# Kernel tuning notes

Hardware: AMD Instinct MI355X
Metric: run time of the kernel (lower is better)

Reference implementation:

```python
import math
import jax, jax.numpy as jnp
import numpy as np

B, S, D, H = 2, 2048, 2048, 16
HD = D // H
EPS = 1e-6


def _precompute_freqs_cis(dim, end, theta=500000.0):
    inv_freqs = 1.0 / theta ** (np.arange(0, dim, 2, dtype=np.float32) / dim)
    t = np.arange(end, dtype=np.float32)
    freqs = np.outer(t, inv_freqs).astype(np.float32)
    # [1, end, 1, dim//2, 2] matching torch stack(cos, sin, dim=4)
    return jnp.asarray(np.stack([np.cos(freqs)[None, :, None, :], np.sin(freqs)[None, :, None, :]], axis=4))


def setup_inputs() -> dict:
    key = jax.random.key(0)
    k1, k2, k3 = jax.random.split(key, 3)
    x = jax.random.normal(k1, (B, S, D), dtype=jnp.float32)
    w_qkv = jax.random.normal(k2, (3 * D, D), dtype=jnp.float32) * 0.02
    w_out = jax.random.normal(k3, (D, D), dtype=jnp.float32) * 0.02
    attn_scale = jnp.asarray(math.log2(S * S - S), dtype=jnp.float32)
    freqs_cis = _precompute_freqs_cis(HD, S)
    return {"x": x, "w_qkv": w_qkv, "w_out": w_out, "attn_scale": attn_scale, "freqs_cis": freqs_cis}


def _apply_rotary(q, k, fc):
    # q, k: [b, s, h, hd]; fc: [1, s, 1, hd//2, 2]
    b, s, h, hd = q.shape
    qk = jnp.concatenate([q, k], axis=2).reshape(b, s, 2 * h, hd // 2, 2)
    real = qk[..., 0] * fc[..., 0] - qk[..., 1] * fc[..., 1]
    imag = qk[..., 1] * fc[..., 0] + qk[..., 0] * fc[..., 1]
    rot = jnp.stack([real, imag], axis=-1).reshape(b, s, 2 * h, hd)
    return rot[:, :, :h], rot[:, :, h:]


def reference(x, w_qkv, w_out, attn_scale, freqs_cis):
    b, s, d = x.shape
    qkv = x @ w_qkv.T                      # [b, s, 3d]
    q, k, v = jnp.split(qkv, 3, axis=2)
    q = q.reshape(b, s, H, HD)
    k = k.reshape(b, s, H, HD)
    v = v.reshape(b, s, H, HD)
    q, k = _apply_rotary(q, k, freqs_cis[:, :s])
    # -> [b, h, s, hd]
    q = q.transpose(0, 2, 1, 3)
    k = k.transpose(0, 2, 1, 3)
    v = v.transpose(0, 2, 1, 3)
    # per-head L2 norm of q/k, learned scale on q
    q = q / (jnp.linalg.norm(q, axis=-1, keepdims=True) + EPS)
    k = k / (jnp.linalg.norm(k, axis=-1, keepdims=True) + EPS)
    q = q * attn_scale
    # causal SDPA with scale=1.0
    scores = jnp.einsum('bhqd,bhkd->bhqk', q, k)
    causal = jnp.tril(jnp.ones((s, s), dtype=bool))
    scores = jnp.where(causal, scores, -jnp.inf)
    attn = jax.nn.softmax(scores, axis=-1)
    out = jnp.einsum('bhqk,bhkd->bhqd', attn, v)
    out = out.transpose(0, 2, 1, 3).reshape(b, s, d)
    return out @ w_out.T
```

## Files before the change

kernel.cpp:

```cpp
#include <hip/hip_runtime.h>
#include <stdint.h>

#define B_  2
#define S_  2048
#define D_  2048
#define H_  16
#define HD_ 128
#define D3_ 6144

typedef unsigned short u16;
typedef __attribute__((ext_vector_type(8))) __bf16 bf16x8;
typedef __attribute__((ext_vector_type(4))) float f32x4;
typedef __attribute__((ext_vector_type(8))) u16  u16x8;
typedef __attribute__((ext_vector_type(4))) u16  u16x4;
typedef __attribute__((ext_vector_type(2))) u16  u16x2;

__device__ inline u16 f2bf(float f) {
  union { float f; uint32_t u; } v; v.f = f;
  uint32_t r = v.u + 0x7FFFu + ((v.u >> 16) & 1u);
  return (u16)(r >> 16);
}
__device__ inline float bf2f(u16 u) {
  union { float f; uint32_t u; } v; v.u = ((uint32_t)u) << 16;
  return v.f;
}
__device__ inline void gload_lds16(const void* g, void* l) {
  __builtin_amdgcn_global_load_lds((const __attribute__((address_space(1))) uint32_t*)g,
                                   (__attribute__((address_space(3))) uint32_t*)l, 16, 0, 0);
}

#define TILE_SYNC() do { \
    asm volatile("s_waitcnt lgkmcnt(0)" ::: "memory"); \
    asm volatile("s_waitcnt vmcnt(0)" ::: "memory"); \
    __builtin_amdgcn_s_barrier(); \
    asm volatile("" ::: "memory"); \
  } while (0)

__global__ __launch_bounds__(256) void castk(const float* __restrict__ in, u16* __restrict__ out, int n) {
  int i = blockIdx.x * 256 + threadIdx.x;
  int n8 = n >> 3;
  if (i < n8) {
    f32x4 a = ((const f32x4*)in)[2*i];
    f32x4 b = ((const f32x4*)in)[2*i + 1];
    u16x8 o;
#pragma unroll
    for (int j = 0; j < 4; ++j) o[j] = f2bf(a[j]);
#pragma unroll
    for (int j = 0; j < 4; ++j) o[4+j] = f2bf(b[j]);
    ((u16x8*)out)[i] = o;
  }
}

template<int BF16OUT>
__global__ __launch_bounds__(512, 2) void gemm8(const u16* __restrict__ A, const u16* __restrict__ Bw,
                                                void* __restrict__ Cp, int M, int N, int K) {
  __shared__ __align__(16) u16 lds_[65536];
  char* ldsb = (char*)lds_;
  const int tid = threadIdx.x;
  const int w = tid >> 6, l = tid & 63;
  const int lr = l & 15, lg = l >> 4;
  const int wr = w >> 2, wc = w & 3;
  const int nbn = (int)gridDim.x;
  const int nwg = nbn * (int)gridDim.y;
  const int bid = (int)(blockIdx.y * gridDim.x + blockIdx.x);
  const int swz = (bid & 7) * (nwg >> 3) + (bid >> 3);
  const int bm = swz / nbn, bn = swz % nbn;

  f32x4 acc[8][4] = {};

  int row4[4], col4[4];
#pragma unroll
  for (int i = 0; i < 4; ++i) {
    int off = i*8192 + tid*16;
    row4[i] = off >> 7;
    col4[i] = (off & 127) ^ ((row4[i] & 7) << 4);
  }
  const size_t rs = (size_t)K * 2;
  const char* Ab = (const char*)A + (size_t)bm * 256 * rs;
  const char* Bb = (const char*)Bw + (size_t)bn * 256 * rs;
  const int wb = w * 1024;

#define STG(T_) do { \
    char* dA_ = ldsb + ((T_)&1)*32768; \
    char* dB_ = ldsb + 65536 + ((T_)&1)*32768; \
    _Pragma("unroll") \
    for (int i_ = 0; i_ < 4; ++i_) \
      gload_lds16(Ab + (size_t)row4[i_]*rs + (size_t)(T_)*128 + col4[i_], dA_ + i_*8192 + wb); \
    _Pragma("unroll") \
    for (int i_ = 0; i_ < 4; ++i_) \
      gload_lds16(Bb + (size_t)row4[i_]*rs + (size_t)(T_)*128 + col4[i_], dB_ + i_*8192 + wb); \
  } while (0)

#define RD_A(dst, mf, ks) do { int row_ = wr*128 + (mf)*16 + lr; \
    dst = *(const bf16x8*)(La + row_*128 + (((ks)*64 + lg*16) ^ ((row_ & 7) << 4))); } while (0)
#define RD_B(dst, nf, ks) do { int row_ = wc*64 + (nf)*16 + lr; \
    dst = *(const bf16x8*)(Lb + row_*128 + (((ks)*64 + lg*16) ^ ((row_ & 7) << 4))); } while (0)

  const int NT = K >> 6;
  STG(0);
  TILE_SYNC();

  for (int T = 0; T < NT; ++T) {
    const char* La = ldsb + (T & 1)*32768;
    const char* Lb = ldsb + 65536 + (T & 1)*32768;
    if (T + 1 < NT) STG(T + 1);

    bf16x8 a0[8], a1[8], b0[4], b1[4];
#pragma unroll
    for (int mf = 0; mf < 8; ++mf) { RD_A(a0[mf], mf, 0); RD_A(a1[mf], mf, 1); }
#pragma unroll
    for (int nf = 0; nf < 4; ++nf) { RD_B(b0[nf], nf, 0); RD_B(b1[nf], nf, 1); }
#pragma unroll
    for (int mf = 0; mf < 8; ++mf)
#pragma unroll
      for (int nf = 0; nf < 4; ++nf)
        acc[mf][nf] = __builtin_amdgcn_mfma_f32_16x16x32_bf16(a0[mf], b0[nf], acc[mf][nf], 0, 0, 0);
#pragma unroll
    for (int mf = 0; mf < 8; ++mf)
#pragma unroll
      for (int nf = 0; nf < 4; ++nf)
        acc[mf][nf] = __builtin_amdgcn_mfma_f32_16x16x32_bf16(a1[mf], b1[nf], acc[mf][nf], 0, 0, 0);
    TILE_SYNC();
  }
#undef STG
#undef RD_A
#undef RD_B

#pragma unroll
  for (int mf = 0; mf < 8; ++mf)
#pragma unroll
    for (int nf = 0; nf < 4; ++nf)
#pragma unroll
      for (int j = 0; j < 4; ++j) {
        int m = bm*256 + wr*128 + mf*16 + lg*4 + j;
        int n = bn*256 + wc*64 + nf*16 + lr;
        float v = acc[mf][nf][j];
        if (BF16OUT) ((u16*)Cp)[(size_t)m * N + n] = f2bf(v);
        else         ((float*)Cp)[(size_t)m * N + n] = v;
      }
}

template<int BF16OUT>
__global__ __launch_bounds__(256, 2) void gemm_bt(const u16* __restrict__ A, const u16* __restrict__ Bw,
                                                  void* __restrict__ Cp, int M, int N, int K) {
  __shared__ __align__(16) u16 lds_[32768];
  char* ldsb = (char*)lds_;
  const int tid = threadIdx.x;
  const int w = tid >> 6, l = tid & 63;
  const int lr = l & 15, lg = l >> 4;
  const int nwg = (int)(gridDim.x * gridDim.y);
  const int bid = (int)(blockIdx.y * gridDim.x + blockIdx.x);
  const int swz = (bid & 7) * (nwg >> 3) + (bid >> 3);
  const int bm = swz / (int)gridDim.x, bn = swz % (int)gridDim.x;
  const int wr = w >> 1, wc = w & 1;

  f32x4 acc[4][4] = {};

  int row4[4], col4[4];
#pragma unroll
  for (int i = 0; i < 4; ++i) {
    int off = i*4096 + tid*16;
    row4[i] = off >> 7;
    col4[i] = (off & 127) ^ ((row4[i] & 7) << 4);
  }
  const size_t rs = (size_t)K * 2;
  const char* Ab = (const char*)A + (size_t)bm * 128 * rs;
  const char* Bb = (const char*)Bw + (size_t)bn * 128 * rs;
  const int wb = w * 1024;

#define STG(T_) do { \
    char* dA_ = ldsb + ((T_)&1)*16384; \
    char* dB_ = ldsb + 32768 + ((T_)&1)*16384; \
    _Pragma("unroll") \
    for (int i_ = 0; i_ < 4; ++i_) \
      gload_lds16(Ab + (size_t)row4[i_]*rs + (size_t)(T_)*128 + col4[i_], dA_ + i_*4096 + wb); \
    _Pragma("unroll") \
    for (int i_ = 0; i_ < 4; ++i_) \
      gload_lds16(Bb + (size_t)row4[i_]*rs + (size_t)(T_)*128 + col4[i_], dB_ + i_*4096 + wb); \
  } while (0)

  const int NT = K >> 6;
  STG(0);
  TILE_SYNC();

  for (int T = 0; T < NT; ++T) {
    const char* La = ldsb + (T & 1)*16384;
    const char* Lb = ldsb + 32768 + (T & 1)*16384;
    if (T + 1 < NT) STG(T + 1);

    bf16x8 af[4][2], bf[4][2];
#pragma unroll
    for (int mt = 0; mt < 4; ++mt) {
      int row = wr*64 + mt*16 + lr;
#pragma unroll
      for (int ks = 0; ks < 2; ++ks)
        af[mt][ks] = *(const bf16x8*)(La + row*128 + ((ks*64 + lg*16) ^ ((row & 7) << 4)));
    }
#pragma unroll
    for (int nt = 0; nt < 4; ++nt) {
      int row = wc*64 + nt*16 + lr;
#pragma unroll
      for (int ks = 0; ks < 2; ++ks)
        bf[nt][ks] = *(const bf16x8*)(Lb + row*128 + ((ks*64 + lg*16) ^ ((row & 7) << 4)));
    }
#pragma unroll
    for (int mt = 0; mt < 4; ++mt)
#pragma unroll
      for (int nt = 0; nt < 4; ++nt)
        acc[mt][nt] = __builtin_amdgcn_mfma_f32_16x16x32_bf16(af[mt][0], bf[nt][0], acc[mt][nt], 0, 0, 0);
#pragma unroll
    for (int mt = 0; mt < 4; ++mt)
#pragma unroll
      for (int nt = 0; nt < 4; ++nt)
        acc[mt][nt] = __builtin_amdgcn_mfma_f32_16x16x32_bf16(af[mt][1], bf[nt][1], acc[mt][nt], 0, 0, 0);
    TILE_SYNC();
  }
#undef STG

#pragma unroll
  for (int mt = 0; mt < 4; ++mt)
#pragma unroll
    for (int nt = 0; nt < 4; ++nt)
#pragma unroll
      for (int j = 0; j < 4; ++j) {
        int m = bm*128 + wr*64 + mt*16 + lg*4 + j;
        int n = bn*128 + wc*64 + nt*16 + lr;
        float v = acc[mt][nt][j];
        if (BF16OUT) ((u16*)Cp)[(size_t)m * N + n] = f2bf(v);
        else         ((float*)Cp)[(size_t)m * N + n] = v;
      }
}

__global__ __launch_bounds__(256) void rope_norm(const u16* __restrict__ qkv, const float* __restrict__ fc,
                                                 const float* __restrict__ scale_p,
                                                 u16* __restrict__ Qo, u16* __restrict__ Ko) {
  int gid = blockIdx.x;
  int bs = gid >> 2;
  int s = bs & (S_ - 1);
  int b = bs >> 11;
  int w = threadIdx.x >> 6, l = threadIdx.x & 63;
  int h = (gid & 3)*4 + w;
  float2 cs = ((const float2*)fc)[(size_t)s*64 + l];
  float scale = scale_p[0] * 1.4426950408889634f;
  const u16* base = qkv + (size_t)bs * D3_;
  size_t obase = ((size_t)(b*H_ + h) * S_ + s) * HD_ + 2*l;
  {
    const u16* p = base + h*HD_ + 2*l;
    float x0 = bf2f(p[0]), x1 = bf2f(p[1]);
    float r0 = x0*cs.x - x1*cs.y;
    float r1 = x1*cs.x + x0*cs.y;
    float t = r0*r0 + r1*r1;
#pragma unroll
    for (int mk = 1; mk < 64; mk <<= 1) t += __shfl_xor(t, mk, 64);
    float inv = scale / (sqrtf(t) + 1e-6f);
    u16x2 o; o[0] = f2bf(r0*inv); o[1] = f2bf(r1*inv);
    *(u16x2*)(Qo + obase) = o;
  }
  {
    const u16* p = base + D_ + h*HD_ + 2*l;
    float x0 = bf2f(p[0]), x1 = bf2f(p[1]);
    float r0 = x0*cs.x - x1*cs.y;
    float r1 = x1*cs.x + x0*cs.y;
    float t = r0*r0 + r1*r1;
#pragma unroll
    for (int mk = 1; mk < 64; mk <<= 1) t += __shfl_xor(t, mk, 64);
    float inv = 1.0f / (sqrtf(t) + 1e-6f);
    u16x2 o; o[0] = f2bf(r0*inv); o[1] = f2bf(r1*inv);
    *(u16x2*)(Ko + obase) = o;
  }
}

__global__ __launch_bounds__(256) void v_trans(const u16* __restrict__ qkv, u16* __restrict__ Vt) {
  __shared__ u16 vt[64][136];
  int blk = blockIdx.x;
  int bh = blk >> 5, st = blk & 31;
  int b = bh >> 4, h = bh & 15;
  int s0 = st * 64;
  int tid = threadIdx.x;
#pragma unroll
  for (int i = 0; i < 4; ++i) {
    int idx = tid + i*256;
    int row = idx >> 4, ch = idx & 15;
    u16x8 v = *(const u16x8*)(qkv + (size_t)(b*S_ + s0 + row) * D3_ + 2*D_ + h*HD_ + ch*8);
    *(u16x8*)(&vt[row][ch*8]) = v;
  }
  __syncthreads();
#pragma unroll
  for (int p = 0; p < 2; ++p) {
    int d = p*64 + (tid >> 2);
    int q = (tid & 3) * 16;
    u16x8 t0, t1;
#pragma unroll
    for (int i = 0; i < 8; ++i) t0[i] = vt[q + i][d];
#pragma unroll
    for (int i = 0; i < 8; ++i) t1[i] = vt[q + 8 + i][d];
    u16* dst = Vt + ((size_t)bh * HD_ + d) * S_ + s0 + q;
    *(u16x8*)dst = t0;
    *(u16x8*)(dst + 8) = t1;
  }
}

__global__ __launch_bounds__(512) void flash_attn(const u16* __restrict__ Qh, const u16* __restrict__ Kh,
                                                  const u16* __restrict__ Vt, u16* __restrict__ AO) {
  __shared__ __align__(16) u16 lK[2][64*128];
  __shared__ __align__(16) u16 lV[128*64];
  __shared__ __align__(16) u16 lP[8][16*72];
  const int i0 = (int)blockIdx.x;
  const int k5 = i0 & 255;
  const int bh = k5 >> 3;
  const int jj = k5 & 7;
  const int qt = (i0 < 256) ? (15 - jj) : jj;
  const int tid = threadIdx.x, w = tid >> 6, l = tid & 63;
  const int lr = l & 15, lg = l >> 4;
  const int b = bh >> 4, h = bh & 15;

  bf16x8 qf[4];
  {
    const u16* qp = Qh + ((size_t)bh * S_ + qt*128 + w*16 + lr) * HD_ + lg*8;
#pragma unroll
    for (int ks = 0; ks < 4; ++ks) qf[ks] = *(const bf16x8*)(qp + ks*32);
  }
  float m0 = -__builtin_inff(), ls0 = 0.f;
  f32x4 oacc[8] = {};

  int krow[2], kcol[2], vrow[2], vcol[2], dstb[2];
#pragma unroll
  for (int p = 0; p < 2; ++p) {
    int off = p*8192 + tid*16;
    krow[p] = off >> 8; kcol[p] = (off & 255) ^ ((krow[p] & 7) << 4);
    vrow[p] = off >> 7; vcol[p] = (off & 127) ^ ((vrow[p] & 7) << 4);
    dstb[p] = p*8192 + w*1024;
  }
  const char* Kb = (const char*)(Kh + (size_t)bh * S_ * HD_);
  const char* Vb = (const char*)(Vt + (size_t)bh * HD_ * S_);

#define STAGE_K(nb, kt_) do {                                                       \
    _Pragma("unroll")                                                               \
    for (int p_ = 0; p_ < 2; ++p_)                                                  \
      gload_lds16(Kb + (size_t)((kt_)*64 + krow[p_])*256 + kcol[p_],                \
                  (char*)lK[nb] + dstb[p_]);                                        \
  } while (0)
#define STAGE_V(kt_) do {                                                           \
    _Pragma("unroll")                                                               \
    for (int p_ = 0; p_ < 2; ++p_)                                                  \
      gload_lds16(Vb + (size_t)vrow[p_]*(S_*2) + (kt_)*128 + vcol[p_],              \
                  (char*)lV + dstb[p_]);                                            \
  } while (0)

  const int nt = 2*qt + 2;
  STAGE_K(0, 0);
  STAGE_V(0);
  int cur = 0;
  for (int kt = 0; kt < nt; ++kt) {
    asm volatile("s_waitcnt vmcnt(2)" ::: "memory");
    __builtin_amdgcn_s_barrier();
    asm volatile("" ::: "memory");
    const char* lKb = (const char*)lK[cur];

    f32x4 sc[4] = {};
    __builtin_amdgcn_s_setprio(1);
#pragma unroll
    for (int ks = 0; ks < 4; ++ks) {
#pragma unroll
      for (int f = 0; f < 4; ++f) {
        int row = f*16 + lr;
        bf16x8 kf = *(const bf16x8*)(lKb + row*256 + ((ks*64 + lg*16) ^ ((row & 7) << 4)));
        sc[f] = __builtin_amdgcn_mfma_f32_16x16x32_bf16(kf, qf[ks], sc[f], 0, 0, 0);
      }
    }
    __builtin_amdgcn_s_setprio(0);
    if (kt < nt-1) STAGE_K(cur ^ 1, kt + 1);

    if (kt >= nt-2) {
#pragma unroll
      for (int f = 0; f < 4; ++f)
#pragma unroll
        for (int j = 0; j < 4; ++j)
          if (kt*64 + f*16 + lg*4 + j > qt*128 + w*16 + lr) sc[f][j] = -__builtin_inff();
    }
    float pmax = sc[0][0];
#pragma unroll
    for (int f = 0; f < 4; ++f)
#pragma unroll
      for (int j = 0; j < 4; ++j) pmax = fmaxf(pmax, sc[f][j]);
    pmax = fmaxf(pmax, __shfl_xor(pmax, 16, 64));
    pmax = fmaxf(pmax, __shfl_xor(pmax, 32, 64));
    float mn = fmaxf(m0, pmax);
    float resc = exp2f(m0 - mn);
    m0 = mn;
    float rsum = 0.f;
#pragma unroll
    for (int f = 0; f < 4; ++f)
#pragma unroll
      for (int j = 0; j < 4; ++j) {
        float p = exp2f(sc[f][j] - mn);
        sc[f][j] = p;
        rsum += p;
      }
    rsum += __shfl_xor(rsum, 16, 64);
    rsum += __shfl_xor(rsum, 32, 64);
    ls0 = ls0 * resc + rsum;
    float rescj[4];
#pragma unroll
    for (int j = 0; j < 4; ++j) rescj[j] = __shfl(resc, lg*4 + j, 64);
#pragma unroll
    for (int fd = 0; fd < 8; ++fd)
#pragma unroll
      for (int j = 0; j < 4; ++j) oacc[fd][j] *= rescj[j];
#pragma unroll
    for (int f = 0; f < 4; ++f) {
      u16x4 pk;
#pragma unroll
      for (int j = 0; j < 4; ++j) pk[j] = f2bf(sc[f][j]);
      *(u16x4*)((char*)lP[w] + lr*144 + f*32 + lg*8) = pk;
    }

    if (kt < nt-1) { asm volatile("s_waitcnt vmcnt(2)" ::: "memory"); }
    else           { asm volatile("s_waitcnt vmcnt(0)" ::: "memory"); }
    __builtin_amdgcn_s_barrier();
    asm volatile("" ::: "memory");
    __builtin_amdgcn_s_setprio(1);
#pragma unroll
    for (int ks = 0; ks < 2; ++ks) {
      bf16x8 pf = *(const bf16x8*)((const char*)lP[w] + lr*144 + ks*64 + lg*16);
#pragma unroll
      for (int fd = 0; fd < 8; ++fd) {
        int row = fd*16 + lr;
        bf16x8 vf = *(const bf16x8*)((const char*)lV + row*128 + ((ks*64 + lg*16) ^ ((row & 7) << 4)));
        oacc[fd] = __builtin_amdgcn_mfma_f32_16x16x32_bf16(pf, vf, oacc[fd], 0, 0, 0);
      }
    }
    __builtin_amdgcn_s_setprio(0);
    asm volatile("" ::: "memory");
    __builtin_amdgcn_s_barrier();
    asm volatile("" ::: "memory");
    if (kt < nt-1) STAGE_V(kt + 1);
    cur ^= 1;
  }
#undef STAGE_K
#undef STAGE_V
  float invl[4];
#pragma unroll
  for (int j = 0; j < 4; ++j) {
    float lsj = __shfl(ls0, lg*4 + j, 64);
    invl[j] = 1.0f / lsj;
  }
#pragma unroll
  for (int fd = 0; fd < 8; ++fd)
#pragma unroll
    for (int j = 0; j < 4; ++j) {
      int qq = qt*128 + w*16 + lg*4 + j;
      int dd = fd*16 + lr;
      float v = oacc[fd][j] * invl[j];
      AO[((size_t)b*S_ + qq)*D_ + h*HD_ + dd] = f2bf(v);
    }
}

extern "C" void kernel_launch(void* const* d_in, const int* in_sizes, int n_in,
                              void* d_out, int out_size, void* d_ws, size_t ws_size,
                              hipStream_t stream) {
  const float* x        = (const float*)d_in[0];
  const float* w_qkv    = (const float*)d_in[1];
  const float* w_out    = (const float*)d_in[2];
  const float* attn_sc  = (const float*)d_in[3];
  const float* freqs    = (const float*)d_in[4];

  if (ws_size < 167772160u) return;

  char* ws = (char*)d_ws;
  u16* xbf  = (u16*)(ws);
  u16* wqbf = (u16*)(ws + 16777216);
  u16* wobf = (u16*)(ws + 41943040);
  u16* qkv  = (u16*)(ws + 50331648);
  u16* Qh   = (u16*)(ws + 100663296);
  u16* Kh   = (u16*)(ws + 117440512);
  u16* Vt   = (u16*)(ws + 134217728);
  u16* AO   = (u16*)(ws + 150994944);

  castk<<<4096, 256, 0, stream>>>(x,     xbf,  8388608);
  castk<<<6144, 256, 0, stream>>>(w_qkv, wqbf, 12582912);
  castk<<<2048, 256, 0, stream>>>(w_out, wobf, 4194304);

  gemm8<1><<<dim3(24, 16), 512, 0, stream>>>(xbf, wqbf, qkv, 4096, 6144, 2048);

  rope_norm<<<16384, 256, 0, stream>>>(qkv, freqs, attn_sc, Qh, Kh);
  v_trans<<<1024, 256, 0, stream>>>(qkv, Vt);

  flash_attn<<<512, 512, 0, stream>>>(Qh, Kh, Vt, AO);

  gemm_bt<0><<<dim3(16, 32), 256, 0, stream>>>(AO, wobf, (float*)d_out, 4096, 2048, 2048);
}
```

Baseline: 278.1 us.

## Give each flash-attention wave two query sub-tiles and split GEMM fragment loads

The flash attention kernel moves from 8 waves of 16 query rows to 4 waves of 32 query rows each, with launch bounds of 256 threads and 2 blocks per CU. Each K and V fragment read from LDS now feeds two MFMAs, which halves LDS traffic per MFMA. The trade is twice the accumulator registers per wave and more load instructions per thread when staging tiles. The GEMMs also interleave the two k-step MFMAs per accumulator, and the large GEMM loads A fragments in two halves to lower register pressure.

```diff
diff --git a/kernel.cpp b/kernel.cpp
--- a/kernel.cpp
+++ b/kernel.cpp
@@ -105,21 +105,27 @@
     const char* Lb = ldsb + 65536 + (T & 1)*32768;
     if (T + 1 < NT) STG(T + 1);
 
-    bf16x8 a0[8], a1[8], b0[4], b1[4];
-#pragma unroll
-    for (int mf = 0; mf < 8; ++mf) { RD_A(a0[mf], mf, 0); RD_A(a1[mf], mf, 1); }
+    bf16x8 a0[4], a1[4], b0[4], b1[4];
+#pragma unroll
+    for (int mf = 0; mf < 4; ++mf) { RD_A(a0[mf], mf, 0); RD_A(a1[mf], mf, 1); }
 #pragma unroll
     for (int nf = 0; nf < 4; ++nf) { RD_B(b0[nf], nf, 0); RD_B(b1[nf], nf, 1); }
 #pragma unroll
-    for (int mf = 0; mf < 8; ++mf)
-#pragma unroll
-      for (int nf = 0; nf < 4; ++nf)
+    for (int mf = 0; mf < 4; ++mf)
+#pragma unroll
+      for (int nf = 0; nf < 4; ++nf) {
         acc[mf][nf] = __builtin_amdgcn_mfma_f32_16x16x32_bf16(a0[mf], b0[nf], acc[mf][nf], 0, 0, 0);
-#pragma unroll
-    for (int mf = 0; mf < 8; ++mf)
-#pragma unroll
-      for (int nf = 0; nf < 4; ++nf)
         acc[mf][nf] = __builtin_amdgcn_mfma_f32_16x16x32_bf16(a1[mf], b1[nf], acc[mf][nf], 0, 0, 0);
+      }
+#pragma unroll
+    for (int mf = 0; mf < 4; ++mf) { RD_A(a0[mf], mf + 4, 0); RD_A(a1[mf], mf + 4, 1); }
+#pragma unroll
+    for (int mf = 0; mf < 4; ++mf)
+#pragma unroll
+      for (int nf = 0; nf < 4; ++nf) {
+        acc[mf+4][nf] = __builtin_amdgcn_mfma_f32_16x16x32_bf16(a0[mf], b0[nf], acc[mf+4][nf], 0, 0, 0);
+        acc[mf+4][nf] = __builtin_amdgcn_mfma_f32_16x16x32_bf16(a1[mf], b1[nf], acc[mf+4][nf], 0, 0, 0);
+      }
     TILE_SYNC();
   }
 #undef STG
@@ -206,13 +212,10 @@
 #pragma unroll
     for (int mt = 0; mt < 4; ++mt)
 #pragma unroll
-      for (int nt = 0; nt < 4; ++nt)
+      for (int nt = 0; nt < 4; ++nt) {
         acc[mt][nt] = __builtin_amdgcn_mfma_f32_16x16x32_bf16(af[mt][0], bf[nt][0], acc[mt][nt], 0, 0, 0);
-#pragma unroll
-    for (int mt = 0; mt < 4; ++mt)
-#pragma unroll
-      for (int nt = 0; nt < 4; ++nt)
         acc[mt][nt] = __builtin_amdgcn_mfma_f32_16x16x32_bf16(af[mt][1], bf[nt][1], acc[mt][nt], 0, 0, 0);
+      }
     TILE_SYNC();
   }
 #undef STG
@@ -300,11 +303,11 @@
   }
 }
 
-__global__ __launch_bounds__(512) void flash_attn(const u16* __restrict__ Qh, const u16* __restrict__ Kh,
-                                                  const u16* __restrict__ Vt, u16* __restrict__ AO) {
+__global__ __launch_bounds__(256, 2) void flash_attn(const u16* __restrict__ Qh, const u16* __restrict__ Kh,
+                                                     const u16* __restrict__ Vt, u16* __restrict__ AO) {
   __shared__ __align__(16) u16 lK[2][64*128];
   __shared__ __align__(16) u16 lV[128*64];
-  __shared__ __align__(16) u16 lP[8][16*72];
+  __shared__ __align__(16) u16 lP[4][32*72];
   const int i0 = (int)blockIdx.x;
   const int k5 = i0 & 255;
   const int bh = k5 >> 3;
@@ -314,35 +317,38 @@
   const int lr = l & 15, lg = l >> 4;
   const int b = bh >> 4, h = bh & 15;
 
-  bf16x8 qf[4];
-  {
-    const u16* qp = Qh + ((size_t)bh * S_ + qt*128 + w*16 + lr) * HD_ + lg*8;
-#pragma unroll
-    for (int ks = 0; ks < 4; ++ks) qf[ks] = *(const bf16x8*)(qp + ks*32);
-  }
-  float m0 = -__builtin_inff(), ls0 = 0.f;
-  f32x4 oacc[8] = {};
-
-  int krow[2], kcol[2], vrow[2], vcol[2], dstb[2];
-#pragma unroll
-  for (int p = 0; p < 2; ++p) {
-    int off = p*8192 + tid*16;
+  bf16x8 qf[2][4];
+#pragma unroll
+  for (int qh = 0; qh < 2; ++qh) {
+    const u16* qp = Qh + ((size_t)bh * S_ + qt*128 + w*32 + qh*16 + lr) * HD_ + lg*8;
+#pragma unroll
+    for (int ks = 0; ks < 4; ++ks) qf[qh][ks] = *(const bf16x8*)(qp + ks*32);
+  }
+  float m0[2], ls0[2];
+  f32x4 oacc[2][8] = {};
+#pragma unroll
+  for (int qh = 0; qh < 2; ++qh) { m0[qh] = -__builtin_inff(); ls0[qh] = 0.f; }
+
+  int krow[4], kcol[4], vrow[4], vcol[4], dstb[4];
+#pragma unroll
+  for (int p = 0; p < 4; ++p) {
+    int off = p*4096 + tid*16;
     krow[p] = off >> 8; kcol[p] = (off & 255) ^ ((krow[p] & 7) << 4);
     vrow[p] = off >> 7; vcol[p] = (off & 127) ^ ((vrow[p] & 7) << 4);
-    dstb[p] = p*8192 + w*1024;
+    dstb[p] = p*4096 + w*1024;
   }
   const char* Kb = (const char*)(Kh + (size_t)bh * S_ * HD_);
   const char* Vb = (const char*)(Vt + (size_t)bh * HD_ * S_);
 
 #define STAGE_K(nb, kt_) do {                                                       \
     _Pragma("unroll")                                                               \
-    for (int p_ = 0; p_ < 2; ++p_)                                                  \
+    for (int p_ = 0; p_ < 4; ++p_)                                                  \
       gload_lds16(Kb + (size_t)((kt_)*64 + krow[p_])*256 + kcol[p_],                \
                   (char*)lK[nb] + dstb[p_]);                                        \
   } while (0)
 #define STAGE_V(kt_) do {                                                           \
     _Pragma("unroll")                                                               \
-    for (int p_ = 0; p_ < 2; ++p_)                                                  \
+    for (int p_ = 0; p_ < 4; ++p_)                                                  \
       gload_lds16(Vb + (size_t)vrow[p_]*(S_*2) + (kt_)*128 + vcol[p_],              \
                   (char*)lV + dstb[p_]);                                            \
   } while (0)
@@ -352,12 +358,12 @@
   STAGE_V(0);
   int cur = 0;
   for (int kt = 0; kt < nt; ++kt) {
-    asm volatile("s_waitcnt vmcnt(2)" ::: "memory");
+    asm volatile("s_waitcnt vmcnt(4)" ::: "memory");
     __builtin_amdgcn_s_barrier();
     asm volatile("" ::: "memory");
     const char* lKb = (const char*)lK[cur];
 
-    f32x4 sc[4] = {};
+    f32x4 sc[2][4] = {};
     __builtin_amdgcn_s_setprio(1);
 #pragma unroll
     for (int ks = 0; ks < 4; ++ks) {
@@ -365,7 +371,8 @@
       for (int f = 0; f < 4; ++f) {
         int row = f*16 + lr;
         bf16x8 kf = *(const bf16x8*)(lKb + row*256 + ((ks*64 + lg*16) ^ ((row & 7) << 4)));
-        sc[f] = __builtin_amdgcn_mfma_f32_16x16x32_bf16(kf, qf[ks], sc[f], 0, 0, 0);
+        sc[0][f] = __builtin_amdgcn_mfma_f32_16x16x32_bf16(kf, qf[0][ks], sc[0][f], 0, 0, 0);
+        sc[1][f] = __builtin_amdgcn_mfma_f32_16x16x32_bf16(kf, qf[1][ks], sc[1][f], 0, 0, 0);
       }
     }
     __builtin_amdgcn_s_setprio(0);
@@ -373,61 +380,68 @@
 
     if (kt >= nt-2) {
 #pragma unroll
+      for (int qh = 0; qh < 2; ++qh)
+#pragma unroll
+        for (int f = 0; f < 4; ++f)
+#pragma unroll
+          for (int j = 0; j < 4; ++j)
+            if (kt*64 + f*16 + lg*4 + j > qt*128 + w*32 + qh*16 + lr) sc[qh][f][j] = -__builtin_inff();
+    }
+#pragma unroll
+    for (int qh = 0; qh < 2; ++qh) {
+      float pmax = sc[qh][0][0];
+#pragma unroll
       for (int f = 0; f < 4; ++f)
 #pragma unroll
-        for (int j = 0; j < 4; ++j)
-          if (kt*64 + f*16 + lg*4 + j > qt*128 + w*16 + lr) sc[f][j] = -__builtin_inff();
-    }
-    float pmax = sc[0][0];
-#pragma unroll
-    for (int f = 0; f < 4; ++f)
-#pragma unroll
-      for (int j = 0; j < 4; ++j) pmax = fmaxf(pmax, sc[f][j]);
-    pmax = fmaxf(pmax, __shfl_xor(pmax, 16, 64));
-    pmax = fmaxf(pmax, __shfl_xor(pmax, 32, 64));
-    float mn = fmaxf(m0, pmax);
-    float resc = exp2f(m0 - mn);
-    m0 = mn;
-    float rsum = 0.f;
-#pragma unroll
-    for (int f = 0; f < 4; ++f)
-#pragma unroll
-      for (int j = 0; j < 4; ++j) {
-        float p = exp2f(sc[f][j] - mn);
-        sc[f][j] = p;
-        rsum += p;
-      }
-    rsum += __shfl_xor(rsum, 16, 64);
-    rsum += __shfl_xor(rsum, 32, 64);
-    ls0 = ls0 * resc + rsum;
-    float rescj[4];
-#pragma unroll
-    for (int j = 0; j < 4; ++j) rescj[j] = __shfl(resc, lg*4 + j, 64);
-#pragma unroll
-    for (int fd = 0; fd < 8; ++fd)
-#pragma unroll
-      for (int j = 0; j < 4; ++j) oacc[fd][j] *= rescj[j];
-#pragma unroll
-    for (int f = 0; f < 4; ++f) {
-      u16x4 pk;
-#pragma unroll
-      for (int j = 0; j < 4; ++j) pk[j] = f2bf(sc[f][j]);
-      *(u16x4*)((char*)lP[w] + lr*144 + f*32 + lg*8) = pk;
-    }
-
-    if (kt < nt-1) { asm volatile("s_waitcnt vmcnt(2)" ::: "memory"); }
+        for (int j = 0; j < 4; ++j) pmax = fmaxf(pmax, sc[qh][f][j]);
+      pmax = fmaxf(pmax, __shfl_xor(pmax, 16, 64));
+      pmax = fmaxf(pmax, __shfl_xor(pmax, 32, 64));
+      float mn = fmaxf(m0[qh], pmax);
+      float resc = exp2f(m0[qh] - mn);
+      m0[qh] = mn;
+      float rsum = 0.f;
+#pragma unroll
+      for (int f = 0; f < 4; ++f)
+#pragma unroll
+        for (int j = 0; j < 4; ++j) {
+          float p = exp2f(sc[qh][f][j] - mn);
+          sc[qh][f][j] = p;
+          rsum += p;
+        }
+      rsum += __shfl_xor(rsum, 16, 64);
+      rsum += __shfl_xor(rsum, 32, 64);
+      ls0[qh] = ls0[qh] * resc + rsum;
+      float rescj[4];
+#pragma unroll
+      for (int j = 0; j < 4; ++j) rescj[j] = __shfl(resc, lg*4 + j, 64);
+#pragma unroll
+      for (int fd = 0; fd < 8; ++fd)
+#pragma unroll
+        for (int j = 0; j < 4; ++j) oacc[qh][fd][j] *= rescj[j];
+#pragma unroll
+      for (int f = 0; f < 4; ++f) {
+        u16x4 pk;
+#pragma unroll
+        for (int j = 0; j < 4; ++j) pk[j] = f2bf(sc[qh][f][j]);
+        *(u16x4*)((char*)lP[w] + (qh*16 + lr)*144 + f*32 + lg*8) = pk;
+      }
+    }
+
+    if (kt < nt-1) { asm volatile("s_waitcnt vmcnt(4)" ::: "memory"); }
     else           { asm volatile("s_waitcnt vmcnt(0)" ::: "memory"); }
     __builtin_amdgcn_s_barrier();
     asm volatile("" ::: "memory");
     __builtin_amdgcn_s_setprio(1);
 #pragma unroll
     for (int ks = 0; ks < 2; ++ks) {
-      bf16x8 pf = *(const bf16x8*)((const char*)lP[w] + lr*144 + ks*64 + lg*16);
+      bf16x8 pf0 = *(const bf16x8*)((const char*)lP[w] + lr*144 + ks*64 + lg*16);
+      bf16x8 pf1 = *(const bf16x8*)((const char*)lP[w] + (16 + lr)*144 + ks*64 + lg*16);
 #pragma unroll
       for (int fd = 0; fd < 8; ++fd) {
         int row = fd*16 + lr;
         bf16x8 vf = *(const bf16x8*)((const char*)lV + row*128 + ((ks*64 + lg*16) ^ ((row & 7) << 4)));
-        oacc[fd] = __builtin_amdgcn_mfma_f32_16x16x32_bf16(pf, vf, oacc[fd], 0, 0, 0);
+        oacc[0][fd] = __builtin_amdgcn_mfma_f32_16x16x32_bf16(pf0, vf, oacc[0][fd], 0, 0, 0);
+        oacc[1][fd] = __builtin_amdgcn_mfma_f32_16x16x32_bf16(pf1, vf, oacc[1][fd], 0, 0, 0);
       }
     }
     __builtin_amdgcn_s_setprio(0);
@@ -439,21 +453,24 @@
   }
 #undef STAGE_K
 #undef STAGE_V
-  float invl[4];
-#pragma unroll
-  for (int j = 0; j < 4; ++j) {
-    float lsj = __shfl(ls0, lg*4 + j, 64);
-    invl[j] = 1.0f / lsj;
-  }
-#pragma unroll
-  for (int fd = 0; fd < 8; ++fd)
+#pragma unroll
+  for (int qh = 0; qh < 2; ++qh) {
+    float invl[4];
 #pragma unroll
     for (int j = 0; j < 4; ++j) {
-      int qq = qt*128 + w*16 + lg*4 + j;
-      int dd = fd*16 + lr;
-      float v = oacc[fd][j] * invl[j];
-      AO[((size_t)b*S_ + qq)*D_ + h*HD_ + dd] = f2bf(v);
-    }
+      float lsj = __shfl(ls0[qh], lg*4 + j, 64);
+      invl[j] = 1.0f / lsj;
+    }
+#pragma unroll
+    for (int fd = 0; fd < 8; ++fd)
+#pragma unroll
+      for (int j = 0; j < 4; ++j) {
+        int qq = qt*128 + w*32 + qh*16 + lg*4 + j;
+        int dd = fd*16 + lr;
+        float v = oacc[qh][fd][j] * invl[j];
+        AO[((size_t)b*S_ + qq)*D_ + h*HD_ + dd] = f2bf(v);
+      }
+  }
 }
 
 extern "C" void kernel_launch(void* const* d_in, const int* in_sizes, int n_in,
@@ -486,7 +503,7 @@
   rope_norm<<<16384, 256, 0, stream>>>(qkv, freqs, attn_sc, Qh, Kh);
   v_trans<<<1024, 256, 0, stream>>>(qkv, Vt);
 
-  flash_attn<<<512, 512, 0, stream>>>(Qh, Kh, Vt, AO);
+  flash_attn<<<512, 256, 0, stream>>>(Qh, Kh, Vt, AO);
 
   gemm_bt<0><<<dim3(16, 32), 256, 0, stream>>>(AO, wobf, (float*)d_out, 4096, 2048, 2048);
 }
```

Result: slower. 286.0 us (+2.8%).

## Retile QKV GEMM to 256x384, fuse casts, lazily rescale attention accumulators

Applied to the files above, without the earlier changes.

The QKV projection GEMM moves from 256x256 tiles with a K-step of 64 to 256x384 tiles with a K-step of 32. That gives exactly 256 workgroups, one per CU, and drops the XOR swizzle from the LDS layout, which may add bank conflicts. The three fp32-to-bf16 cast launches are merged into one kernel, and the MFMA pair in the output GEMM is interleaved per tile. Flash attention skips rescaling the running output and sum when every lane's new max exceeds the old one by at most 8 in log2 units. That saves shuffles and multiplies, but partial sums can grow by up to a factor of 2^8.

```diff
diff --git a/kernel.cpp b/kernel.cpp
--- a/kernel.cpp
+++ b/kernel.cpp
@@ -36,25 +36,29 @@
     asm volatile("" ::: "memory"); \
   } while (0)
 
-__global__ __launch_bounds__(256) void castk(const float* __restrict__ in, u16* __restrict__ out, int n) {
-  int i = blockIdx.x * 256 + threadIdx.x;
-  int n8 = n >> 3;
-  if (i < n8) {
-    f32x4 a = ((const f32x4*)in)[2*i];
-    f32x4 b = ((const f32x4*)in)[2*i + 1];
-    u16x8 o;
-#pragma unroll
-    for (int j = 0; j < 4; ++j) o[j] = f2bf(a[j]);
-#pragma unroll
-    for (int j = 0; j < 4; ++j) o[4+j] = f2bf(b[j]);
-    ((u16x8*)out)[i] = o;
-  }
+__global__ __launch_bounds__(256) void castk3(const float* __restrict__ x, const float* __restrict__ wq,
+                                              const float* __restrict__ wo,
+                                              u16* __restrict__ xo, u16* __restrict__ wqo, u16* __restrict__ woo) {
+  int blk = (int)blockIdx.x;
+  const float* in; u16* out; int base;
+  if (blk < 4096)       { in = x;  out = xo;  base = blk; }
+  else if (blk < 10240) { in = wq; out = wqo; base = blk - 4096; }
+  else                  { in = wo; out = woo; base = blk - 10240; }
+  int i = base * 256 + (int)threadIdx.x;
+  f32x4 a = ((const f32x4*)in)[2*i];
+  f32x4 b = ((const f32x4*)in)[2*i + 1];
+  u16x8 o;
+#pragma unroll
+  for (int j = 0; j < 4; ++j) o[j] = f2bf(a[j]);
+#pragma unroll
+  for (int j = 0; j < 4; ++j) o[4+j] = f2bf(b[j]);
+  ((u16x8*)out)[i] = o;
 }
 
 template<int BF16OUT>
-__global__ __launch_bounds__(512, 2) void gemm8(const u16* __restrict__ A, const u16* __restrict__ Bw,
-                                                void* __restrict__ Cp, int M, int N, int K) {
-  __shared__ __align__(16) u16 lds_[65536];
+__global__ __launch_bounds__(512, 2) void gemm384(const u16* __restrict__ A, const u16* __restrict__ Bw,
+                                                  void* __restrict__ Cp, int M, int N, int K) {
+  __shared__ __align__(16) u16 lds_[40960];
   char* ldsb = (char*)lds_;
   const int tid = threadIdx.x;
   const int w = tid >> 6, l = tid & 63;
@@ -66,74 +70,64 @@
   const int swz = (bid & 7) * (nwg >> 3) + (bid >> 3);
   const int bm = swz / nbn, bn = swz % nbn;
 
-  f32x4 acc[8][4] = {};
-
-  int row4[4], col4[4];
-#pragma unroll
-  for (int i = 0; i < 4; ++i) {
-    int off = i*8192 + tid*16;
-    row4[i] = off >> 7;
-    col4[i] = (off & 127) ^ ((row4[i] & 7) << 4);
-  }
+  f32x4 acc[8][6] = {};
+
+  int mA[2], kA[2], mB[3], kB[3];
+#pragma unroll
+  for (int p = 0; p < 2; ++p) { int off = p*8192 + tid*16; mA[p] = off >> 6; kA[p] = off & 63; }
+#pragma unroll
+  for (int p = 0; p < 3; ++p) { int off = p*8192 + tid*16; mB[p] = off >> 6; kB[p] = off & 63; }
   const size_t rs = (size_t)K * 2;
   const char* Ab = (const char*)A + (size_t)bm * 256 * rs;
-  const char* Bb = (const char*)Bw + (size_t)bn * 256 * rs;
+  const char* Bb = (const char*)Bw + (size_t)bn * 384 * rs;
   const int wb = w * 1024;
 
 #define STG(T_) do { \
-    char* dA_ = ldsb + ((T_)&1)*32768; \
-    char* dB_ = ldsb + 65536 + ((T_)&1)*32768; \
+    char* dA_ = ldsb + ((T_)&1)*16384; \
+    char* dB_ = ldsb + 32768 + ((T_)&1)*24576; \
     _Pragma("unroll") \
-    for (int i_ = 0; i_ < 4; ++i_) \
-      gload_lds16(Ab + (size_t)row4[i_]*rs + (size_t)(T_)*128 + col4[i_], dA_ + i_*8192 + wb); \
+    for (int p_ = 0; p_ < 2; ++p_) \
+      gload_lds16(Ab + (size_t)mA[p_]*rs + (size_t)(T_)*64 + kA[p_], dA_ + p_*8192 + wb); \
     _Pragma("unroll") \
-    for (int i_ = 0; i_ < 4; ++i_) \
-      gload_lds16(Bb + (size_t)row4[i_]*rs + (size_t)(T_)*128 + col4[i_], dB_ + i_*8192 + wb); \
+    for (int p_ = 0; p_ < 3; ++p_) \
+      gload_lds16(Bb + (size_t)mB[p_]*rs + (size_t)(T_)*64 + kB[p_], dB_ + p_*8192 + wb); \
   } while (0)
 
-#define RD_A(dst, mf, ks) do { int row_ = wr*128 + (mf)*16 + lr; \
-    dst = *(const bf16x8*)(La + row_*128 + (((ks)*64 + lg*16) ^ ((row_ & 7) << 4))); } while (0)
-#define RD_B(dst, nf, ks) do { int row_ = wc*64 + (nf)*16 + lr; \
-    dst = *(const bf16x8*)(Lb + row_*128 + (((ks)*64 + lg*16) ^ ((row_ & 7) << 4))); } while (0)
-
-  const int NT = K >> 6;
+  const int NT = K >> 5;
   STG(0);
   TILE_SYNC();
 
   for (int T = 0; T < NT; ++T) {
-    const char* La = ldsb + (T & 1)*32768;
-    const char* Lb = ldsb + 65536 + (T & 1)*32768;
+    const char* La = ldsb + (T & 1)*16384;
+    const char* Lb = ldsb + 32768 + (T & 1)*24576;
     if (T + 1 < NT) STG(T + 1);
 
-    bf16x8 a0[8], a1[8], b0[4], b1[4];
-#pragma unroll
-    for (int mf = 0; mf < 8; ++mf) { RD_A(a0[mf], mf, 0); RD_A(a1[mf], mf, 1); }
-#pragma unroll
-    for (int nf = 0; nf < 4; ++nf) { RD_B(b0[nf], nf, 0); RD_B(b1[nf], nf, 1); }
-#pragma unroll
-    for (int mf = 0; mf < 8; ++mf)
-#pragma unroll
-      for (int nf = 0; nf < 4; ++nf)
-        acc[mf][nf] = __builtin_amdgcn_mfma_f32_16x16x32_bf16(a0[mf], b0[nf], acc[mf][nf], 0, 0, 0);
-#pragma unroll
-    for (int mf = 0; mf < 8; ++mf)
-#pragma unroll
-      for (int nf = 0; nf < 4; ++nf)
-        acc[mf][nf] = __builtin_amdgcn_mfma_f32_16x16x32_bf16(a1[mf], b1[nf], acc[mf][nf], 0, 0, 0);
+    bf16x8 bfr[6];
+#pragma unroll
+    for (int nf = 0; nf < 6; ++nf) {
+      int row = wc*96 + nf*16 + lr;
+      bfr[nf] = *(const bf16x8*)(Lb + row*64 + lg*16);
+    }
+#pragma unroll
+    for (int mf = 0; mf < 8; ++mf) {
+      int row = wr*128 + mf*16 + lr;
+      bf16x8 af = *(const bf16x8*)(La + row*64 + lg*16);
+#pragma unroll
+      for (int nf = 0; nf < 6; ++nf)
+        acc[mf][nf] = __builtin_amdgcn_mfma_f32_16x16x32_bf16(af, bfr[nf], acc[mf][nf], 0, 0, 0);
+    }
     TILE_SYNC();
   }
 #undef STG
-#undef RD_A
-#undef RD_B
 
 #pragma unroll
   for (int mf = 0; mf < 8; ++mf)
 #pragma unroll
-    for (int nf = 0; nf < 4; ++nf)
+    for (int nf = 0; nf < 6; ++nf)
 #pragma unroll
       for (int j = 0; j < 4; ++j) {
         int m = bm*256 + wr*128 + mf*16 + lg*4 + j;
-        int n = bn*256 + wc*64 + nf*16 + lr;
+        int n = bn*384 + wc*96 + nf*16 + lr;
         float v = acc[mf][nf][j];
         if (BF16OUT) ((u16*)Cp)[(size_t)m * N + n] = f2bf(v);
         else         ((float*)Cp)[(size_t)m * N + n] = v;
@@ -206,13 +200,10 @@
 #pragma unroll
     for (int mt = 0; mt < 4; ++mt)
 #pragma unroll
-      for (int nt = 0; nt < 4; ++nt)
+      for (int nt = 0; nt < 4; ++nt) {
         acc[mt][nt] = __builtin_amdgcn_mfma_f32_16x16x32_bf16(af[mt][0], bf[nt][0], acc[mt][nt], 0, 0, 0);
-#pragma unroll
-    for (int mt = 0; mt < 4; ++mt)
-#pragma unroll
-      for (int nt = 0; nt < 4; ++nt)
         acc[mt][nt] = __builtin_amdgcn_mfma_f32_16x16x32_bf16(af[mt][1], bf[nt][1], acc[mt][nt], 0, 0, 0);
+      }
     TILE_SYNC();
   }
 #undef STG
@@ -385,9 +376,16 @@
       for (int j = 0; j < 4; ++j) pmax = fmaxf(pmax, sc[f][j]);
     pmax = fmaxf(pmax, __shfl_xor(pmax, 16, 64));
     pmax = fmaxf(pmax, __shfl_xor(pmax, 32, 64));
-    float mn = fmaxf(m0, pmax);
-    float resc = exp2f(m0 - mn);
-    m0 = mn;
+    const int norescale = __all(pmax - m0 <= 8.0f);
+    float mn;
+    float resc = 0.f;
+    if (norescale) {
+      mn = m0;
+    } else {
+      mn = fmaxf(m0, pmax);
+      resc = exp2f(m0 - mn);
+      m0 = mn;
+    }
     float rsum = 0.f;
 #pragma unroll
     for (int f = 0; f < 4; ++f)
@@ -399,14 +397,18 @@
       }
     rsum += __shfl_xor(rsum, 16, 64);
     rsum += __shfl_xor(rsum, 32, 64);
-    ls0 = ls0 * resc + rsum;
-    float rescj[4];
-#pragma unroll
-    for (int j = 0; j < 4; ++j) rescj[j] = __shfl(resc, lg*4 + j, 64);
-#pragma unroll
-    for (int fd = 0; fd < 8; ++fd)
-#pragma unroll
-      for (int j = 0; j < 4; ++j) oacc[fd][j] *= rescj[j];
+    if (norescale) {
+      ls0 = ls0 + rsum;
+    } else {
+      ls0 = ls0 * resc + rsum;
+      float rescj[4];
+#pragma unroll
+      for (int j = 0; j < 4; ++j) rescj[j] = __shfl(resc, lg*4 + j, 64);
+#pragma unroll
+      for (int fd = 0; fd < 8; ++fd)
+#pragma unroll
+        for (int j = 0; j < 4; ++j) oacc[fd][j] *= rescj[j];
+    }
 #pragma unroll
     for (int f = 0; f < 4; ++f) {
       u16x4 pk;
@@ -477,11 +479,9 @@
   u16* Vt   = (u16*)(ws + 134217728);
   u16* AO   = (u16*)(ws + 150994944);
 
-  castk<<<4096, 256, 0, stream>>>(x,     xbf,  8388608);
-  castk<<<6144, 256, 0, stream>>>(w_qkv, wqbf, 12582912);
-  castk<<<2048, 256, 0, stream>>>(w_out, wobf, 4194304);
-
-  gemm8<1><<<dim3(24, 16), 512, 0, stream>>>(xbf, wqbf, qkv, 4096, 6144, 2048);
+  castk3<<<12288, 256, 0, stream>>>(x, w_qkv, w_out, xbf, wqbf, wobf);
+
+  gemm384<1><<<dim3(16, 16), 512, 0, stream>>>(xbf, wqbf, qkv, 4096, 6144, 2048);
 
   rope_norm<<<16384, 256, 0, stream>>>(qkv, freqs, attn_sc, Qh, Kh);
   v_trans<<<1024, 256, 0, stream>>>(qkv, Vt);
```

Result: faster. 251.3 us (-9.6%).
